# Performance work log

Hardware: AMD Instinct MI355X
Metric: run time of the kernel (lower is better)

## Reference

```python
import jax, jax.numpy as jnp
import numpy as np

D_MODEL, N_HEADS, N_GROUPS, BASE = 2048, 32, 8, 10000
HEAD_DIM = D_MODEL // N_HEADS  # 64


def _rope_cache(seq, head_dim, base=BASE):
    half = head_dim // 2
    theta = 1.0 / (base ** (jnp.arange(0, head_dim, 2)[:half].astype(jnp.float32) / head_dim))
    ang = jnp.einsum('i,j->ij', jnp.arange(seq, dtype=jnp.float32), theta)  # (seq, half)
    return jnp.cos(ang), jnp.sin(ang)


def _apply_rope(x):
    # x: (b, s, h, head_dim) -> interleaved-pair rotation, matching torch module
    b, s, h, hd = x.shape
    cos, sin = _rope_cache(s, hd)
    xr = x.reshape(b, s, h, hd // 2, 2)
    c = cos[None, :, None, :]
    sn = sin[None, :, None, :]
    x0, x1 = xr[..., 0], xr[..., 1]
    out = jnp.stack((x0 * c - x1 * sn, x1 * c + x0 * sn), axis=-1)
    return out.reshape(b, s, h, hd).astype(x.dtype)


def setup_inputs() -> dict:
    key = jax.random.key(0)
    ks = jax.random.split(key, 8)
    B, S = 1, 2048
    kv_dim = HEAD_DIM * N_GROUPS
    return {
        'Q': jax.random.normal(ks[0], (B, S, D_MODEL), jnp.float32),
        'K': jax.random.normal(ks[1], (B, S, D_MODEL), jnp.float32),
        'V': jax.random.normal(ks[2], (B, S, D_MODEL), jnp.float32),
        'attention_mask': jnp.ones((B, S), jnp.int32),
        'Wq': jax.random.normal(ks[3], (D_MODEL, D_MODEL), jnp.float32) * 0.02,
        'Wk': jax.random.normal(ks[4], (D_MODEL, kv_dim), jnp.float32) * 0.02,
        'Wv': jax.random.normal(ks[5], (D_MODEL, kv_dim), jnp.float32) * 0.02,
        'Wo': jax.random.normal(ks[6], (D_MODEL, D_MODEL), jnp.float32) * 0.02,
        'bo': jnp.zeros((D_MODEL,), jnp.float32),
    }


def reference(Q, K, V, attention_mask, Wq, Wk, Wv, Wo, bo):
    b, s, _ = Q.shape
    g, hpg, hd = N_GROUPS, N_HEADS // N_GROUPS, HEAD_DIM
    # projections (weights stored as [in, out], equivalent to torch x @ W.T)
    q = (Q @ Wq).reshape(b, s, N_HEADS, hd)
    q = _apply_rope(q).reshape(b, s, g, hpg, hd)
    k = _apply_rope((K @ Wk).reshape(b, s, g, hd))
    v = (V @ Wv).reshape(b, s, g, hd)

    scale = jnp.sqrt(jnp.float32(hd))
    scores = jnp.einsum('bnghd,bmgd->bnghm', q, k) / scale  # (b, s, g, hpg, s)
    # padding mask (b, 1, 1, 1, s) and causal mask (1, s, 1, 1, s)
    pad = (attention_mask != 0)[:, None, None, None, :]
    causal = jnp.tril(jnp.ones((s, s), bool))[None, :, None, None, :]
    scores = jnp.where(pad & causal, scores, -jnp.inf)
    attn = jax.nn.softmax(scores, axis=-1)  # dropout p=0.0 -> identity
    out = jnp.einsum('bnghm,bmgd->bnghd', attn, v).reshape(b, s, D_MODEL)
    return out @ Wo + bo
```

## Files before the change

kernel.cpp:

```cpp
#include <hip/hip_runtime.h>

typedef __bf16 bf16_t;
typedef __bf16 bf16x8 __attribute__((ext_vector_type(8)));
typedef __bf16 bf16x4 __attribute__((ext_vector_type(4)));
typedef __bf16 bf16x2 __attribute__((ext_vector_type(2)));
typedef float  f32x4  __attribute__((ext_vector_type(4)));

#define LOG2E 1.44269504088896340736f

__global__ __launch_bounds__(256) void rope_table_k(float* __restrict__ cs,
                                                    float* __restrict__ sn, int S) {
  int i = blockIdx.x * 256 + threadIdx.x;
  if (i >= S * 32) return;
  int s = i >> 5, j = i & 31;
  float theta = powf(10000.0f, -(float)j * (1.0f / 32.0f));
  float a = (float)s * theta;
  cs[i] = cosf(a);
  sn[i] = sinf(a);
}

__global__ void transpose_cast_k(const float* __restrict__ in, bf16_t* __restrict__ out,
                                 int R, int C) {
  __shared__ float tile[32][33];
  int c0 = blockIdx.x * 32, r0 = blockIdx.y * 32;
  int tx = threadIdx.x, ty = threadIdx.y;
  #pragma unroll
  for (int k = 0; k < 32; k += 8)
    tile[ty + k][tx] = in[(size_t)(r0 + ty + k) * C + c0 + tx];
  __syncthreads();
  #pragma unroll
  for (int k = 0; k < 32; k += 8)
    out[(size_t)(c0 + ty + k) * R + r0 + tx] = (bf16_t)tile[tx][ty + k];
}

template<int AF32>
__global__ __launch_bounds__(256) void gemm2_k(
    const void* __restrict__ Aq, const void* __restrict__ Ak, const void* __restrict__ Av,
    const bf16_t* __restrict__ Bq, const bf16_t* __restrict__ Bk, const bf16_t* __restrict__ Bv,
    const int K, const int N, const int mode,
    const float* __restrict__ cs, const float* __restrict__ sn,
    bf16_t* __restrict__ oq, bf16_t* __restrict__ okg, bf16_t* __restrict__ ovt,
    float* __restrict__ ofp, const float* __restrict__ bias, const int S) {
  __shared__ bf16_t a_lds[64][72];
  __shared__ bf16_t b_lds[128][72];
  const int tid = threadIdx.x;
  const int wid = tid >> 6, lane = tid & 63;
  const int fr = lane & 15, kg = lane >> 4;

  const int cb = blockIdx.x, rb = blockIdx.y;
  const void* Ap; const bf16_t* Bp; int emode, col0;
  if (mode == 3) { Ap = Aq; Bp = Bq; emode = 3; col0 = cb * 128; }
  else if (cb < 16) { Ap = Aq; Bp = Bq; emode = 0; col0 = cb * 128; }
  else if (cb < 20) { Ap = Ak; Bp = Bk; emode = 1; col0 = (cb - 16) * 128; }
  else              { Ap = Av; Bp = Bv; emode = 2; col0 = (cb - 20) * 128; }
  const int row0 = rb * 64;
  const int wr = (wid >> 1) * 32, wc = (wid & 1) * 64;

  f32x4 acc[2][4];
  #pragma unroll
  for (int i = 0; i < 2; ++i)
    #pragma unroll
    for (int j = 0; j < 4; ++j)
      acc[i][j] = (f32x4){0.f, 0.f, 0.f, 0.f};

  const int ra = tid >> 2, sa = (tid & 3) * 16;
  const int rbv = tid >> 1, sb = (tid & 1) * 32;

  float4 fa0, fa1, fa2, fa3;
  bf16x8 a0, a1;
  bf16x8 b0, b1, b2, b3;

  const float* Af = (const float*)Ap;
  const bf16_t* Ab = (const bf16_t*)Ap;

#define LOADA(kt)                                                              \
  do {                                                                         \
    if (AF32) {                                                                \
      const float* p = &Af[(size_t)(row0 + ra) * K + (kt) + sa];               \
      fa0 = *(const float4*)(p);      fa1 = *(const float4*)(p + 4);           \
      fa2 = *(const float4*)(p + 8);  fa3 = *(const float4*)(p + 12);          \
    } else {                                                                   \
      const bf16_t* p = &Ab[(size_t)(row0 + ra) * K + (kt) + sa];              \
      a0 = *(const bf16x8*)(p); a1 = *(const bf16x8*)(p + 8);                  \
    }                                                                          \
    const bf16_t* q = &Bp[(size_t)(col0 + rbv) * K + (kt) + sb];               \
    b0 = *(const bf16x8*)(q);      b1 = *(const bf16x8*)(q + 8);               \
    b2 = *(const bf16x8*)(q + 16); b3 = *(const bf16x8*)(q + 24);              \
  } while (0)

  LOADA(0);

  for (int kt = 0; kt < K; kt += 64) {
    __syncthreads();
    if (AF32) {
      bf16x8 w0, w1;
      w0[0]=(bf16_t)fa0.x; w0[1]=(bf16_t)fa0.y; w0[2]=(bf16_t)fa0.z; w0[3]=(bf16_t)fa0.w;
      w0[4]=(bf16_t)fa1.x; w0[5]=(bf16_t)fa1.y; w0[6]=(bf16_t)fa1.z; w0[7]=(bf16_t)fa1.w;
      w1[0]=(bf16_t)fa2.x; w1[1]=(bf16_t)fa2.y; w1[2]=(bf16_t)fa2.z; w1[3]=(bf16_t)fa2.w;
      w1[4]=(bf16_t)fa3.x; w1[5]=(bf16_t)fa3.y; w1[6]=(bf16_t)fa3.z; w1[7]=(bf16_t)fa3.w;
      *(bf16x8*)&a_lds[ra][sa] = w0;
      *(bf16x8*)&a_lds[ra][sa + 8] = w1;
    } else {
      *(bf16x8*)&a_lds[ra][sa] = a0;
      *(bf16x8*)&a_lds[ra][sa + 8] = a1;
    }
    *(bf16x8*)&b_lds[rbv][sb]      = b0;
    *(bf16x8*)&b_lds[rbv][sb + 8]  = b1;
    *(bf16x8*)&b_lds[rbv][sb + 16] = b2;
    *(bf16x8*)&b_lds[rbv][sb + 24] = b3;
    __syncthreads();
    if (kt + 64 < K) LOADA(kt + 64);
    #pragma unroll
    for (int ks = 0; ks < 2; ++ks) {
      bf16x8 af[2], bfr[4];
      #pragma unroll
      for (int mi = 0; mi < 2; ++mi) af[mi]  = *(const bf16x8*)&a_lds[wr + mi * 16 + fr][ks * 32 + kg * 8];
      #pragma unroll
      for (int ni = 0; ni < 4; ++ni) bfr[ni] = *(const bf16x8*)&b_lds[wc + ni * 16 + fr][ks * 32 + kg * 8];
      #pragma unroll
      for (int mi = 0; mi < 2; ++mi)
        #pragma unroll
        for (int ni = 0; ni < 4; ++ni)
          acc[mi][ni] = __builtin_amdgcn_mfma_f32_16x16x32_bf16(af[mi], bfr[ni], acc[mi][ni], 0, 0, 0);
    }
  }
#undef LOADA

  #pragma unroll
  for (int mi = 0; mi < 2; ++mi) {
    #pragma unroll
    for (int ni = 0; ni < 4; ++ni) {
      #pragma unroll
      for (int r = 0; r < 4; ++r) {
        const int grow = row0 + wr + mi * 16 + kg * 4 + r;
        const int gcol = col0 + wc + ni * 16 + fr;
        float v = acc[mi][ni][r];
        if (emode == 3) {
          ofp[(size_t)grow * N + gcol] = v + bias[gcol];
        } else if (emode == 2) {
          const int gi = gcol >> 6, d = gcol & 63;
          ovt[((size_t)gi * 64 + d) * S + grow] = (bf16_t)v;
        } else {
          const float pv = __shfl_xor(v, 1);
          const int d = gcol & 63, p = d >> 1, hh = gcol >> 6;
          const float c = cs[grow * 32 + p], s = sn[grow * 32 + p];
          float o = (d & 1) ? fmaf(pv, s, v * c) : fmaf(-pv, s, v * c);
          if (emode == 0) {
            o *= 0.125f * LOG2E;
            oq[((size_t)hh * S + grow) * 64 + d] = (bf16_t)o;
          } else {
            okg[((size_t)hh * S + grow) * 64 + d] = (bf16_t)o;
          }
        }
      }
    }
  }
}

__device__ __forceinline__ int swz8(int r, int c) { return r * 64 + (((c) ^ (r & 7)) << 3); }

__global__ __launch_bounds__(256) void attn_k(
    const bf16_t* __restrict__ qh,
    const bf16_t* __restrict__ kgr,
    const bf16_t* __restrict__ vtg,
    const int* __restrict__ amask,
    bf16_t* __restrict__ ao,
    const int S) {
  __shared__ bf16_t k_lds[64 * 64];
  __shared__ bf16_t vt_lds[64 * 64];
  __shared__ bf16_t p_lds[4][16 * 64];
  const int tid = threadIdx.x, wid = tid >> 6, lane = tid & 63;
  const int fr = lane & 15, kgp = lane >> 4;
  const int h = blockIdx.x, g = h >> 2;
  const int qb = 31 - blockIdx.y;
  const int q0 = qb * 64 + wid * 16;
  const int qg = q0 + fr;

  const bf16_t* qbase = qh + ((size_t)h * S + q0 + fr) * 64;
  const bf16x8 qf0 = *(const bf16x8*)&qbase[kgp * 8];
  const bf16x8 qf1 = *(const bf16x8*)&qbase[32 + kgp * 8];

  f32x4 oacc[4];
  #pragma unroll
  for (int t = 0; t < 4; ++t) oacc[t] = (f32x4){0.f, 0.f, 0.f, 0.f};
  float m_ = -1e30f, l_ = 0.f;

  const int srow = tid >> 2, sc4 = tid & 3;
  const bf16_t* kbase = kgr + (size_t)g * S * 64;
  const bf16_t* vbase = vtg + (size_t)g * 64 * S;
  const int cmax = qb + 1;

  bf16x8 nk0 = *(const bf16x8*)&kbase[(size_t)srow * 64 + sc4 * 8];
  bf16x8 nk1 = *(const bf16x8*)&kbase[(size_t)srow * 64 + 32 + sc4 * 8];
  bf16x8 nv0 = *(const bf16x8*)&vbase[(size_t)srow * S + sc4 * 8];
  bf16x8 nv1 = *(const bf16x8*)&vbase[(size_t)srow * S + 32 + sc4 * 8];
  int mvc = amask[lane];
  *(bf16x8*)&k_lds[swz8(srow, sc4)]      = nk0;
  *(bf16x8*)&k_lds[swz8(srow, 4 + sc4)]  = nk1;
  *(bf16x8*)&vt_lds[swz8(srow, sc4)]     = nv0;
  *(bf16x8*)&vt_lds[swz8(srow, 4 + sc4)] = nv1;
  __syncthreads();

  for (int c = 0; c < cmax; ++c) {
    const int kc0 = c * 64;
    const unsigned long long pm = __ballot(mvc == 0);
    const bool more = (c + 1 < cmax);
    if (more) {
      const int kc1 = kc0 + 64;
      nk0 = *(const bf16x8*)&kbase[(size_t)(kc1 + srow) * 64 + sc4 * 8];
      nk1 = *(const bf16x8*)&kbase[(size_t)(kc1 + srow) * 64 + 32 + sc4 * 8];
      nv0 = *(const bf16x8*)&vbase[(size_t)srow * S + kc1 + sc4 * 8];
      nv1 = *(const bf16x8*)&vbase[(size_t)srow * S + kc1 + 32 + sc4 * 8];
      mvc = amask[kc1 + lane];
    }

    f32x4 sc[4];
    #pragma unroll
    for (int a = 0; a < 4; ++a) {
      const bf16x8 ka0 = *(const bf16x8*)&k_lds[swz8(a * 16 + fr, kgp)];
      const bf16x8 ka1 = *(const bf16x8*)&k_lds[swz8(a * 16 + fr, 4 + kgp)];
      f32x4 z = (f32x4){0.f, 0.f, 0.f, 0.f};
      z = __builtin_amdgcn_mfma_f32_16x16x32_bf16(ka0, qf0, z, 0, 0, 0);
      z = __builtin_amdgcn_mfma_f32_16x16x32_bf16(ka1, qf1, z, 0, 0, 0);
      sc[a] = z;
    }

    if (c == qb) {
      #pragma unroll
      for (int a = 0; a < 4; ++a)
        #pragma unroll
        for (int r = 0; r < 4; ++r) {
          const int kl = a * 16 + 4 * kgp + r;
          if (kc0 + kl > qg) sc[a][r] = -1e30f;
        }
    }
    if (pm) {
      #pragma unroll
      for (int a = 0; a < 4; ++a)
        #pragma unroll
        for (int r = 0; r < 4; ++r) {
          const int kl = a * 16 + 4 * kgp + r;
          if ((pm >> kl) & 1) sc[a][r] = -1e30f;
        }
    }

    float smax = sc[0][0];
    #pragma unroll
    for (int a = 0; a < 4; ++a)
      #pragma unroll
      for (int r = 0; r < 4; ++r) smax = fmaxf(smax, sc[a][r]);
    smax = fmaxf(smax, __shfl_xor(smax, 16));
    smax = fmaxf(smax, __shfl_xor(smax, 32));
    const float mn = fmaxf(m_, smax);
    const float al = exp2f(m_ - mn);
    float ps = 0.f;
    #pragma unroll
    for (int a = 0; a < 4; ++a)
      #pragma unroll
      for (int r = 0; r < 4; ++r) {
        const float p = exp2f(sc[a][r] - mn);
        sc[a][r] = p;
        ps += p;
      }
    ps += __shfl_xor(ps, 16);
    ps += __shfl_xor(ps, 32);
    l_ = l_ * al + ps;
    m_ = mn;
    #pragma unroll
    for (int t = 0; t < 4; ++t)
      #pragma unroll
      for (int r = 0; r < 4; ++r) oacc[t][r] *= al;

    #pragma unroll
    for (int a = 0; a < 4; ++a)
      #pragma unroll
      for (int j = 0; j < 2; ++j) {
        bf16x2 w;
        w[0] = (bf16_t)sc[a][2 * j];
        w[1] = (bf16_t)sc[a][2 * j + 1];
        const int off = a * 16 + 4 * kgp + 2 * j;
        *(bf16x2*)&p_lds[wid][fr * 64 + (((off >> 3) ^ (fr & 7)) << 3) + (off & 7)] = w;
      }
    const bf16x8 pa0 = *(const bf16x8*)&p_lds[wid][swz8(fr, kgp)];
    const bf16x8 pa1 = *(const bf16x8*)&p_lds[wid][swz8(fr, 4 + kgp)];

    #pragma unroll
    for (int t = 0; t < 4; ++t) {
      const bf16x8 vb0 = *(const bf16x8*)&vt_lds[swz8(t * 16 + fr, kgp)];
      const bf16x8 vb1 = *(const bf16x8*)&vt_lds[swz8(t * 16 + fr, 4 + kgp)];
      oacc[t] = __builtin_amdgcn_mfma_f32_16x16x32_bf16(vb0, pa0, oacc[t], 0, 0, 0);
      oacc[t] = __builtin_amdgcn_mfma_f32_16x16x32_bf16(vb1, pa1, oacc[t], 0, 0, 0);
    }

    if (more) {
      __syncthreads();
      *(bf16x8*)&k_lds[swz8(srow, sc4)]      = nk0;
      *(bf16x8*)&k_lds[swz8(srow, 4 + sc4)]  = nk1;
      *(bf16x8*)&vt_lds[swz8(srow, sc4)]     = nv0;
      *(bf16x8*)&vt_lds[swz8(srow, 4 + sc4)] = nv1;
      __syncthreads();
    }
  }

  const float inv = 1.0f / l_;
  #pragma unroll
  for (int t = 0; t < 4; ++t) {
    bf16x4 o4;
    #pragma unroll
    for (int r = 0; r < 4; ++r) o4[r] = (bf16_t)(oacc[t][r] * inv);
    *(bf16x4*)&ao[(size_t)(q0 + fr) * 2048 + h * 64 + t * 16 + 4 * kgp] = o4;
  }
}

extern "C" void kernel_launch(void* const* d_in, const int* in_sizes, int n_in,
                              void* d_out, int out_size, void* d_ws, size_t ws_size,
                              hipStream_t stream) {
  const float* Q  = (const float*)d_in[0];
  const float* K  = (const float*)d_in[1];
  const float* V  = (const float*)d_in[2];
  const int*   am = (const int*)d_in[3];
  const float* Wq = (const float*)d_in[4];
  const float* Wk = (const float*)d_in[5];
  const float* Wv = (const float*)d_in[6];
  const float* Wo = (const float*)d_in[7];
  const float* bo = (const float*)d_in[8];
  float* out = (float*)d_out;

  const int S = 2048, D = 2048, KV = 512;
  char* w = (char*)d_ws;
  const size_t MB = 1u << 20;
  bf16_t* WqT = (bf16_t*)(w + 0 * MB);
  bf16_t* WkT = (bf16_t*)(w + 8 * MB);
  bf16_t* WvT = (bf16_t*)(w + 10 * MB);
  bf16_t* WoT = (bf16_t*)(w + 12 * MB);
  bf16_t* qh  = (bf16_t*)(w + 20 * MB);
  bf16_t* kgr = (bf16_t*)(w + 28 * MB);
  bf16_t* vtg = (bf16_t*)(w + 30 * MB);
  bf16_t* ao  = (bf16_t*)(w + 32 * MB);
  float*  cs  = (float*)(w + 40 * MB);
  float*  sn  = (float*)(w + 40 * MB + 256 * 1024);

  rope_table_k<<<256, 256, 0, stream>>>(cs, sn, S);
  dim3 tb(32, 8);
  transpose_cast_k<<<dim3(64, 64), tb, 0, stream>>>(Wq, WqT, D, D);
  transpose_cast_k<<<dim3(16, 64), tb, 0, stream>>>(Wk, WkT, D, KV);
  transpose_cast_k<<<dim3(16, 64), tb, 0, stream>>>(Wv, WvT, D, KV);
  transpose_cast_k<<<dim3(64, 64), tb, 0, stream>>>(Wo, WoT, D, D);

  gemm2_k<1><<<dim3(24, 32), 256, 0, stream>>>(Q, K, V, WqT, WkT, WvT, D, D, 5,
                                               cs, sn, qh, kgr, vtg, nullptr, nullptr, S);

  attn_k<<<dim3(32, 32), 256, 0, stream>>>(qh, kgr, vtg, am, ao, S);

  gemm2_k<0><<<dim3(16, 32), 256, 0, stream>>>(ao, nullptr, nullptr, WoT, nullptr, nullptr,
                                               D, D, 3, nullptr, nullptr, nullptr, nullptr,
                                               nullptr, out, bo, S);
}
```

Baseline: 167.7 us.

## Pre-cast activations to bf16 and add XCD-aware block swizzle to GEMMs

Adds a separate cast kernel that converts Q, K and V from fp32 to bf16 up front, so the projection GEMM reads bf16 A tiles instead of fp32 and converting them in its inner loop. The GEMM becomes non-templated with a 1D grid, and block indices are remapped so consecutive tiles land on the same XCD for better L2 reuse. The cost is an extra pass that reads fp32 and writes bf16 activations, plus more workspace.

```diff
diff --git a/kernel.cpp b/kernel.cpp
--- a/kernel.cpp
+++ b/kernel.cpp
@@ -19,6 +19,26 @@
   sn[i] = sinf(a);
 }
 
+__global__ __launch_bounds__(256) void cast3_k(const float* __restrict__ A,
+                                               const float* __restrict__ B,
+                                               const float* __restrict__ C,
+                                               bf16_t* __restrict__ oa,
+                                               bf16_t* __restrict__ ob,
+                                               bf16_t* __restrict__ oc) {
+  const int b = blockIdx.x;
+  const float* in; bf16_t* out;
+  if (b < 2048) { in = A; out = oa; }
+  else if (b < 4096) { in = B; out = ob; }
+  else { in = C; out = oc; }
+  const int j = (b & 2047) * 256 + threadIdx.x;
+  const float4 v0 = *(const float4*)&in[(size_t)j * 8];
+  const float4 v1 = *(const float4*)&in[(size_t)j * 8 + 4];
+  bf16x8 o;
+  o[0]=(bf16_t)v0.x; o[1]=(bf16_t)v0.y; o[2]=(bf16_t)v0.z; o[3]=(bf16_t)v0.w;
+  o[4]=(bf16_t)v1.x; o[5]=(bf16_t)v1.y; o[6]=(bf16_t)v1.z; o[7]=(bf16_t)v1.w;
+  *(bf16x8*)&out[(size_t)j * 8] = o;
+}
+
 __global__ void transpose_cast_k(const float* __restrict__ in, bf16_t* __restrict__ out,
                                  int R, int C) {
   __shared__ float tile[32][33];
@@ -33,22 +53,29 @@
     out[(size_t)(c0 + ty + k) * R + r0 + tx] = (bf16_t)tile[tx][ty + k];
 }
 
-template<int AF32>
+__device__ __forceinline__ int xcd_swz(int bid, int nb) {
+  const int q = nb >> 3, r = nb & 7;
+  const int xcd = bid & 7, idx = bid >> 3;
+  return (xcd < r ? xcd * (q + 1) : r * (q + 1) + (xcd - r) * q) + idx;
+}
+
 __global__ __launch_bounds__(256) void gemm2_k(
-    const void* __restrict__ Aq, const void* __restrict__ Ak, const void* __restrict__ Av,
+    const bf16_t* __restrict__ Aq, const bf16_t* __restrict__ Ak, const bf16_t* __restrict__ Av,
     const bf16_t* __restrict__ Bq, const bf16_t* __restrict__ Bk, const bf16_t* __restrict__ Bv,
     const int K, const int N, const int mode,
     const float* __restrict__ cs, const float* __restrict__ sn,
     bf16_t* __restrict__ oq, bf16_t* __restrict__ okg, bf16_t* __restrict__ ovt,
-    float* __restrict__ ofp, const float* __restrict__ bias, const int S) {
+    float* __restrict__ ofp, const float* __restrict__ bias, const int S,
+    const int ncb, const int nb) {
   __shared__ bf16_t a_lds[64][72];
   __shared__ bf16_t b_lds[128][72];
   const int tid = threadIdx.x;
   const int wid = tid >> 6, lane = tid & 63;
   const int fr = lane & 15, kg = lane >> 4;
 
-  const int cb = blockIdx.x, rb = blockIdx.y;
-  const void* Ap; const bf16_t* Bp; int emode, col0;
+  const int lin = xcd_swz(blockIdx.x, nb);
+  const int cb = lin % ncb, rb = lin / ncb;
+  const bf16_t* Ap; const bf16_t* Bp; int emode, col0;
   if (mode == 3) { Ap = Aq; Bp = Bq; emode = 3; col0 = cb * 128; }
   else if (cb < 16) { Ap = Aq; Bp = Bq; emode = 0; col0 = cb * 128; }
   else if (cb < 20) { Ap = Ak; Bp = Bk; emode = 1; col0 = (cb - 16) * 128; }
@@ -66,23 +93,12 @@
   const int ra = tid >> 2, sa = (tid & 3) * 16;
   const int rbv = tid >> 1, sb = (tid & 1) * 32;
 
-  float4 fa0, fa1, fa2, fa3;
-  bf16x8 a0, a1;
-  bf16x8 b0, b1, b2, b3;
-
-  const float* Af = (const float*)Ap;
-  const bf16_t* Ab = (const bf16_t*)Ap;
+  bf16x8 a0, a1, b0, b1, b2, b3;
 
 #define LOADA(kt)                                                              \
   do {                                                                         \
-    if (AF32) {                                                                \
-      const float* p = &Af[(size_t)(row0 + ra) * K + (kt) + sa];               \
-      fa0 = *(const float4*)(p);      fa1 = *(const float4*)(p + 4);           \
-      fa2 = *(const float4*)(p + 8);  fa3 = *(const float4*)(p + 12);          \
-    } else {                                                                   \
-      const bf16_t* p = &Ab[(size_t)(row0 + ra) * K + (kt) + sa];              \
-      a0 = *(const bf16x8*)(p); a1 = *(const bf16x8*)(p + 8);                  \
-    }                                                                          \
+    const bf16_t* p = &Ap[(size_t)(row0 + ra) * K + (kt) + sa];                \
+    a0 = *(const bf16x8*)(p); a1 = *(const bf16x8*)(p + 8);                    \
     const bf16_t* q = &Bp[(size_t)(col0 + rbv) * K + (kt) + sb];               \
     b0 = *(const bf16x8*)(q);      b1 = *(const bf16x8*)(q + 8);               \
     b2 = *(const bf16x8*)(q + 16); b3 = *(const bf16x8*)(q + 24);              \
@@ -92,18 +108,8 @@
 
   for (int kt = 0; kt < K; kt += 64) {
     __syncthreads();
-    if (AF32) {
-      bf16x8 w0, w1;
-      w0[0]=(bf16_t)fa0.x; w0[1]=(bf16_t)fa0.y; w0[2]=(bf16_t)fa0.z; w0[3]=(bf16_t)fa0.w;
-      w0[4]=(bf16_t)fa1.x; w0[5]=(bf16_t)fa1.y; w0[6]=(bf16_t)fa1.z; w0[7]=(bf16_t)fa1.w;
-      w1[0]=(bf16_t)fa2.x; w1[1]=(bf16_t)fa2.y; w1[2]=(bf16_t)fa2.z; w1[3]=(bf16_t)fa2.w;
-      w1[4]=(bf16_t)fa3.x; w1[5]=(bf16_t)fa3.y; w1[6]=(bf16_t)fa3.z; w1[7]=(bf16_t)fa3.w;
-      *(bf16x8*)&a_lds[ra][sa] = w0;
-      *(bf16x8*)&a_lds[ra][sa + 8] = w1;
-    } else {
-      *(bf16x8*)&a_lds[ra][sa] = a0;
-      *(bf16x8*)&a_lds[ra][sa + 8] = a1;
-    }
+    *(bf16x8*)&a_lds[ra][sa]      = a0;
+    *(bf16x8*)&a_lds[ra][sa + 8]  = a1;
     *(bf16x8*)&b_lds[rbv][sb]      = b0;
     *(bf16x8*)&b_lds[rbv][sb + 8]  = b1;
     *(bf16x8*)&b_lds[rbv][sb + 16] = b2;
@@ -330,29 +336,33 @@
   char* w = (char*)d_ws;
   const size_t MB = 1u << 20;
   bf16_t* WqT = (bf16_t*)(w + 0 * MB);
-  bf16_t* WkT = (bf16_t*)(w + 8 * MB);
-  bf16_t* WvT = (bf16_t*)(w + 10 * MB);
-  bf16_t* WoT = (bf16_t*)(w + 12 * MB);
+  bf16_t* WoT = (bf16_t*)(w + 8 * MB);
+  bf16_t* WkT = (bf16_t*)(w + 16 * MB);
+  bf16_t* WvT = (bf16_t*)(w + 18 * MB);
   bf16_t* qh  = (bf16_t*)(w + 20 * MB);
   bf16_t* kgr = (bf16_t*)(w + 28 * MB);
   bf16_t* vtg = (bf16_t*)(w + 30 * MB);
   bf16_t* ao  = (bf16_t*)(w + 32 * MB);
-  float*  cs  = (float*)(w + 40 * MB);
-  float*  sn  = (float*)(w + 40 * MB + 256 * 1024);
+  bf16_t* Qb  = (bf16_t*)(w + 40 * MB);
+  bf16_t* Kb  = (bf16_t*)(w + 48 * MB);
+  bf16_t* Vb  = (bf16_t*)(w + 56 * MB);
+  float*  cs  = (float*)(w + 64 * MB);
+  float*  sn  = (float*)(w + 64 * MB + 256 * 1024);
 
   rope_table_k<<<256, 256, 0, stream>>>(cs, sn, S);
+  cast3_k<<<6144, 256, 0, stream>>>(Q, K, V, Qb, Kb, Vb);
   dim3 tb(32, 8);
   transpose_cast_k<<<dim3(64, 64), tb, 0, stream>>>(Wq, WqT, D, D);
   transpose_cast_k<<<dim3(16, 64), tb, 0, stream>>>(Wk, WkT, D, KV);
   transpose_cast_k<<<dim3(16, 64), tb, 0, stream>>>(Wv, WvT, D, KV);
   transpose_cast_k<<<dim3(64, 64), tb, 0, stream>>>(Wo, WoT, D, D);
 
-  gemm2_k<1><<<dim3(24, 32), 256, 0, stream>>>(Q, K, V, WqT, WkT, WvT, D, D, 5,
-                                               cs, sn, qh, kgr, vtg, nullptr, nullptr, S);
+  gemm2_k<<<768, 256, 0, stream>>>(Qb, Kb, Vb, WqT, WkT, WvT, D, D, 5,
+                                   cs, sn, qh, kgr, vtg, nullptr, nullptr, S, 24, 768);
 
   attn_k<<<dim3(32, 32), 256, 0, stream>>>(qh, kgr, vtg, am, ao, S);
 
-  gemm2_k<0><<<dim3(16, 32), 256, 0, stream>>>(ao, nullptr, nullptr, WoT, nullptr, nullptr,
-                                               D, D, 3, nullptr, nullptr, nullptr, nullptr,
-                                               nullptr, out, bo, S);
-}
+  gemm2_k<<<512, 256, 0, stream>>>(ao, nullptr, nullptr, WoT, nullptr, nullptr,
+                                   D, D, 3, nullptr, nullptr, nullptr, nullptr,
+                                   nullptr, out, bo, S, 16, 512);
+}
```

After: 162.1 us. -3.3%, faster.
